# Performance work log

Measured on AMD Instinct MI355X. Metric: run time of the kernel, lower is better.

## Reference

```python
import jax, jax.numpy as jnp
import numpy as np

B, N, CIN, COUT = 4, 4096, 64, 64

def setup_inputs() -> dict:
    key = jax.random.key(0)
    k1, k2, k3, k4, k5 = jax.random.split(key, 5)
    X = jax.random.normal(k1, (B, N, CIN), dtype=jnp.float32)
    A = jax.random.uniform(k2, (N, N), dtype=jnp.float32)
    weight1 = jax.random.normal(k3, (CIN, COUT), dtype=jnp.float32) * 0.05
    weight2 = jax.random.normal(k4, (1 * COUT, COUT), dtype=jnp.float32) * 0.05
    alpha = jax.random.normal(k5, (2 * COUT, 1), dtype=jnp.float32) * 0.05
    return {"X": X, "A": A, "weight1": weight1, "weight2": weight2, "alpha": alpha}

def reference(X, A, weight1, weight2, alpha):
    n = A.shape[0]
    c = weight1.shape[1]
    b = X.shape[0]
    # add self loops on the adjacency diagonal
    idx = jnp.arange(n)
    adj = A.at[idx, idx].set(1.0)
    # node transform: [B,N,C]
    out = jnp.matmul(X, weight1)
    # edge feature (P=1): [N,N,1], row-normalized over j (axis=1)
    E = adj[:, :, None]
    E_wave = E / E.sum(axis=1, keepdims=True)
    # attention scores via rank-1 decomposition of alpha
    att_l = jnp.matmul(out, alpha[:c])   # [B,N,1]
    att_r = jnp.matmul(out, alpha[c:])   # [B,N,1]
    scores = jax.nn.leaky_relu(att_l @ jnp.swapaxes(att_r, 1, 2))  # [B,N,N]
    # exp + edge-feature weighting: [P,B,N,N]
    att = jnp.einsum('bij,ijp->pbij', jnp.exp(scores), E_wave)
    # manual softmax-style normalization over neighbors j
    att = att / att.sum(axis=-1, keepdims=True)
    # aggregate: [B,N,P,C] -> [B,N,P*C]
    agg = jnp.einsum('pbij,bjc->bipc', att, out).reshape(b, n, -1)
    return jnp.matmul(agg, weight2)
```

## Files before the change

kernel.cpp:

```cpp
#include <hip/hip_runtime.h>
#include <hip/hip_bf16.h>

typedef __attribute__((ext_vector_type(8))) short short8;
typedef __attribute__((ext_vector_type(4))) float floatx4;

#define NN 4096

static __device__ __forceinline__ unsigned f2bf_rne(float x) {
    union { float f; unsigned u; } v; v.f = x;
    unsigned r = v.u + 0x7fffu + ((v.u >> 16) & 1u);
    return r >> 16;
}
static __device__ __forceinline__ float bf2f(unsigned hi) {
    union { unsigned u; float f; } v; v.u = hi << 16; return v.f;
}

__global__ __launch_bounds__(256, 4)
void prep_kernel(const float* __restrict__ X,
                 const float* __restrict__ W1,
                 const float* __restrict__ W2,
                 const float* __restrict__ alpha,
                 unsigned short* __restrict__ Gt,
                 float* __restrict__ lv,
                 float* __restrict__ rv) {
    __shared__ __align__(16) char sm[53248];
    float* W1s  = (float*)sm;
    float* W2s  = (float*)(sm + 17408);
    float* Wcst = (float*)(sm + 34816);
    float* w1s  = (float*)(sm + 52224);
    float* als  = (float*)(sm + 52736);
    float* GsT  = (float*)sm;

    const int t = threadIdx.x;
    const int row0 = blockIdx.x * 64;
    const int b = row0 >> 12, n0 = row0 & (NN - 1);
    const int w = t >> 6, lane = t & 63;
    const int m = lane & 15, q = lane >> 4;

    const int row = row0 + w * 16 + m;
    const float* xp = X + (size_t)row * 64;
    float4 x0 = *(const float4*)(xp + q * 8);
    float4 x1 = *(const float4*)(xp + q * 8 + 4);
    float4 x2 = *(const float4*)(xp + 32 + q * 8);
    float4 x3 = *(const float4*)(xp + 32 + q * 8 + 4);

    #pragma unroll
    for (int s = 0; s < 4; ++s) {
        int idx = s * 1024 + t * 4;
        int r = idx >> 6, cc = idx & 63;
        *(float4*)&W1s[r * 68 + cc] = *(const float4*)(W1 + idx);
        *(float4*)&W2s[r * 68 + cc] = *(const float4*)(W2 + idx);
    }
    if (t < 128) als[t] = alpha[t];
    __syncthreads();

    {
        const int k = t >> 2, nq = t & 3;
        float acc[16];
        #pragma unroll
        for (int i = 0; i < 16; ++i) acc[i] = 0.f;
        for (int mm = 0; mm < 64; ++mm) {
            float w1v = W1s[k * 68 + mm];
            #pragma unroll
            for (int i = 0; i < 16; ++i)
                acc[i] += w1v * W2s[mm * 68 + nq * 16 + i];
        }
        #pragma unroll
        for (int i = 0; i < 16; ++i)
            Wcst[(nq * 16 + i) * 68 + k] = acc[i];
    }
    if (t < 64) {
        float sl = 0.f, sr = 0.f;
        for (int cc2 = 0; cc2 < 64; ++cc2) {
            float wv = W1s[t * 68 + cc2];
            sl += wv * als[cc2];
            sr += wv * als[64 + cc2];
        }
        w1s[t] = sl; w1s[64 + t] = sr;
    }
    __syncthreads();

    const float xs[16] = {x0.x,x0.y,x0.z,x0.w, x1.x,x1.y,x1.z,x1.w,
                          x2.x,x2.y,x2.z,x2.w, x3.x,x3.y,x3.z,x3.w};

    float pl = 0.f, pr = 0.f;
    #pragma unroll
    for (int ks = 0; ks < 2; ++ks)
        #pragma unroll
        for (int j = 0; j < 8; ++j) {
            int k = ks * 32 + q * 8 + j;
            float xv = xs[ks * 8 + j];
            pl += xv * w1s[k];
            pr += xv * w1s[64 + k];
        }
    pl += __shfl_xor(pl, 16, 64); pl += __shfl_xor(pl, 32, 64);
    pr += __shfl_xor(pr, 16, 64); pr += __shfl_xor(pr, 32, 64);
    if (q == 0) { lv[row] = pl; rv[row] = pr; }

    short8 ah[2], al[2];
    #pragma unroll
    for (int ks = 0; ks < 2; ++ks)
        #pragma unroll
        for (int j = 0; j < 8; ++j) {
            float f = xs[ks * 8 + j];
            unsigned hb = f2bf_rne(f);
            float res = f - bf2f(hb);
            ah[ks][j] = (short)hb;
            al[ks][j] = (short)f2bf_rne(res);
        }

    short8 bfr[4][2];
    #pragma unroll
    for (int nt = 0; nt < 4; ++nt)
        #pragma unroll
        for (int ks = 0; ks < 2; ++ks) {
            const float* wp = &Wcst[(nt * 16 + m) * 68 + ks * 32 + q * 8];
            float4 w0 = *(const float4*)wp;
            float4 w1 = *(const float4*)(wp + 4);
            short8 bf;
            bf[0] = (short)f2bf_rne(w0.x); bf[1] = (short)f2bf_rne(w0.y);
            bf[2] = (short)f2bf_rne(w0.z); bf[3] = (short)f2bf_rne(w0.w);
            bf[4] = (short)f2bf_rne(w1.x); bf[5] = (short)f2bf_rne(w1.y);
            bf[6] = (short)f2bf_rne(w1.z); bf[7] = (short)f2bf_rne(w1.w);
            bfr[nt][ks] = bf;
        }

    floatx4 acc[4] = {{0,0,0,0},{0,0,0,0},{0,0,0,0},{0,0,0,0}};
    #pragma unroll
    for (int ks = 0; ks < 2; ++ks)
        #pragma unroll
        for (int nt = 0; nt < 4; ++nt) {
            acc[nt] = __builtin_amdgcn_mfma_f32_16x16x32_bf16(ah[ks], bfr[nt][ks], acc[nt], 0, 0, 0);
            acc[nt] = __builtin_amdgcn_mfma_f32_16x16x32_bf16(al[ks], bfr[nt][ks], acc[nt], 0, 0, 0);
        }

    __syncthreads();
    #pragma unroll
    for (int nt = 0; nt < 4; ++nt)
        #pragma unroll
        for (int rg = 0; rg < 4; ++rg)
            GsT[(nt * 16 + m) * 68 + w * 16 + q * 4 + rg] = acc[nt][rg];
    __syncthreads();
    unsigned* Gu = (unsigned*)Gt;
    #pragma unroll
    for (int it2 = 0; it2 < 8; ++it2) {
        int c2 = (t >> 5) + it2 * 8;
        int np = t & 31;
        unsigned lo = f2bf_rne(GsT[c2 * 68 + 2 * np]);
        unsigned hi = f2bf_rne(GsT[c2 * 68 + 2 * np + 1]);
        Gu[(((((size_t)(b * 64 + c2)) << 12) + n0) >> 1) + np] = lo | (hi << 16);
    }
}

__global__ __launch_bounds__(1024, 4)
void attn_kernel(const float* __restrict__ A,
                 const unsigned short* __restrict__ Gt,
                 const float* __restrict__ lv,
                 const float* __restrict__ rv,
                 float* __restrict__ out) {
    __shared__ __align__(16) char sm[57600];
    float* rs = (float*)sm;
    float* lis = (float*)(sm + 16384);
    unsigned short* Es = (unsigned short*)(sm + 16640);
    unsigned short* Gs = (unsigned short*)(sm + 37120);

    const int bx = blockIdx.x;
    const int i0 = (bx & 63) * 64;
    const int b  = bx >> 6;
    const int t = threadIdx.x;
    const int wave = t >> 6, lane = t & 63;
    const int grp = wave >> 2, wsub = wave & 3;
    const int m = lane & 15, q = lane >> 4;
    const int irow = wsub * 16 + (lane >> 2);
    const int jseg = lane & 3;

    *(float4*)&rs[t * 4] = *(const float4*)(rv + b * NN + t * 4);
    if (t < 64) lis[t] = lv[b * NN + i0 + t] * 1.44269504f;

    const float* aRow = A + (size_t)(i0 + irow) * NN + grp * 1024 + jseg * 8;
    const unsigned short* gRow = Gt + (((size_t)(b * 64 + irow)) << 12) + grp * 1024 + jseg * 8;
    const int jd = (i0 + irow) - grp * 1024;
    const bool diag_grp = (((i0 + irow) >> 10) == grp);

    unsigned short* EsG = Es + grp * 2560;
    unsigned short* GsG = Gs + grp * 2560;

    float4 a0A = *(const float4*)(aRow);
    float4 a1A = *(const float4*)(aRow + 4);
    uint4  gA  = *(const uint4*)(gRow);
    float4 a0B = *(const float4*)(aRow + 32);
    float4 a1B = *(const float4*)(aRow + 36);
    uint4  gB  = *(const uint4*)(gRow + 32);

    __syncthreads();
    const float li = lis[irow];

    floatx4 acc0 = {0,0,0,0}, acc1 = {0,0,0,0}, acc2 = {0,0,0,0},
            acc3 = {0,0,0,0}, accd = {0,0,0,0};
    short8 ones;
    #pragma unroll
    for (int e = 0; e < 8; ++e) ones[e] = (short)0x3F80;

    auto genE = [&](float4 a0, float4 a1, int chunk) -> uint4 {
        const int jl = chunk * 32 + jseg * 8;
        float aa[8] = {a0.x, a0.y, a0.z, a0.w, a1.x, a1.y, a1.z, a1.w};
        if (diag_grp && (jd >> 5) == chunk) {
            const int dd = jd - jl;
            #pragma unroll
            for (int e = 0; e < 8; ++e) if (dd == e) aa[e] = 1.0f;
        }
        const float4 r0 = *(const float4*)&rs[grp * 1024 + jl];
        const float4 r1 = *(const float4*)&rs[grp * 1024 + jl + 4];
        const float rr[8] = {r0.x, r0.y, r0.z, r0.w, r1.x, r1.y, r1.z, r1.w};
        unsigned ew[4];
        #pragma unroll
        for (int e2 = 0; e2 < 4; ++e2) {
            float s0 = li * rr[2 * e2], s1 = li * rr[2 * e2 + 1];
            s0 = fmaxf(s0, 0.01f * s0);
            s1 = fmaxf(s1, 0.01f * s1);
            float e0 = exp2f(s0) * aa[2 * e2];
            float e1 = exp2f(s1) * aa[2 * e2 + 1];
            ew[e2] = __builtin_amdgcn_perm(__float_as_uint(e1) + 0x8000u,
                                           __float_as_uint(e0) + 0x8000u, 0x07060302u);
        }
        return uint4{ew[0], ew[1], ew[2], ew[3]};
    };

    const int eoff = irow * 40 + jseg * 8;
    for (int c = 0; c < 32; c += 2) {
        uint4 eA = genE(a0A, a1A, c);
        uint4 gsvA = gA;
        { int jn = (c + 2 < 32) ? (c + 2) * 32 : c * 32;
          a0A = *(const float4*)(aRow + jn);
          a1A = *(const float4*)(aRow + jn + 4);
          gA  = *(const uint4*)(gRow + jn); }
        __syncthreads();
        *(uint4*)&EsG[eoff] = eA;
        *(uint4*)&GsG[eoff] = gsvA;
        __syncthreads();
        {
            short8 afr = *(const short8*)&EsG[(wsub * 16 + m) * 40 + q * 8];
            short8 b0  = *(const short8*)&GsG[(m)      * 40 + q * 8];
            short8 b1  = *(const short8*)&GsG[(16 + m) * 40 + q * 8];
            short8 b2  = *(const short8*)&GsG[(32 + m) * 40 + q * 8];
            short8 b3  = *(const short8*)&GsG[(48 + m) * 40 + q * 8];
            acc0 = __builtin_amdgcn_mfma_f32_16x16x32_bf16(afr, b0, acc0, 0, 0, 0);
            acc1 = __builtin_amdgcn_mfma_f32_16x16x32_bf16(afr, b1, acc1, 0, 0, 0);
            acc2 = __builtin_amdgcn_mfma_f32_16x16x32_bf16(afr, b2, acc2, 0, 0, 0);
            acc3 = __builtin_amdgcn_mfma_f32_16x16x32_bf16(afr, b3, acc3, 0, 0, 0);
            accd = __builtin_amdgcn_mfma_f32_16x16x32_bf16(afr, ones, accd, 0, 0, 0);
        }
        uint4 eB = genE(a0B, a1B, c + 1);
        uint4 gsvB = gB;
        { int jn = (c + 3 < 32) ? (c + 3) * 32 : (c + 1) * 32;
          a0B = *(const float4*)(aRow + jn);
          a1B = *(const float4*)(aRow + jn + 4);
          gB  = *(const uint4*)(gRow + jn); }
        __syncthreads();
        *(uint4*)&EsG[eoff] = eB;
        *(uint4*)&GsG[eoff] = gsvB;
        __syncthreads();
        {
            short8 afr = *(const short8*)&EsG[(wsub * 16 + m) * 40 + q * 8];
            short8 b0  = *(const short8*)&GsG[(m)      * 40 + q * 8];
            short8 b1  = *(const short8*)&GsG[(16 + m) * 40 + q * 8];
            short8 b2  = *(const short8*)&GsG[(32 + m) * 40 + q * 8];
            short8 b3  = *(const short8*)&GsG[(48 + m) * 40 + q * 8];
            acc0 = __builtin_amdgcn_mfma_f32_16x16x32_bf16(afr, b0, acc0, 0, 0, 0);
            acc1 = __builtin_amdgcn_mfma_f32_16x16x32_bf16(afr, b1, acc1, 0, 0, 0);
            acc2 = __builtin_amdgcn_mfma_f32_16x16x32_bf16(afr, b2, acc2, 0, 0, 0);
            acc3 = __builtin_amdgcn_mfma_f32_16x16x32_bf16(afr, b3, acc3, 0, 0, 0);
            accd = __builtin_amdgcn_mfma_f32_16x16x32_bf16(afr, ones, accd, 0, 0, 0);
        }
    }

    __syncthreads();
    float* red = (float*)sm;
    const int il = t >> 4, c4 = t & 15;
    float4 osum = {0.f, 0.f, 0.f, 0.f};
    float dsum = 0.f;
    #pragma unroll
    for (int pass = 0; pass < 2; ++pass) {
        if ((grp >> 1) == pass) {
            float* rp_ = red + (grp & 1) * 4352;
            #pragma unroll
            for (int nt = 0; nt < 4; ++nt) {
                floatx4 av = nt == 0 ? acc0 : nt == 1 ? acc1 : nt == 2 ? acc2 : acc3;
                #pragma unroll
                for (int rg = 0; rg < 4; ++rg)
                    rp_[(wsub * 16 + q * 4 + rg) * 68 + nt * 16 + m] = av[rg];
            }
            if (m == 0) {
                #pragma unroll
                for (int rg = 0; rg < 4; ++rg)
                    rp_[(wsub * 16 + q * 4 + rg) * 68 + 64] = accd[rg];
            }
        }
        __syncthreads();
        {
            float4 v0 = *(const float4*)&red[il * 68 + c4 * 4];
            float4 v1 = *(const float4*)&red[4352 + il * 68 + c4 * 4];
            osum.x += v0.x + v1.x; osum.y += v0.y + v1.y;
            osum.z += v0.z + v1.z; osum.w += v0.w + v1.w;
            dsum += red[il * 68 + 64] + red[4352 + il * 68 + 64];
        }
        __syncthreads();
    }
    const float rinv = 1.0f / dsum;
    float4 o;
    o.x = osum.x * rinv; o.y = osum.y * rinv;
    o.z = osum.z * rinv; o.w = osum.w * rinv;
    *(float4*)(out + (((size_t)(b * NN + i0 + il)) << 6) + c4 * 4) = o;
}

extern "C" void kernel_launch(void* const* d_in, const int* in_sizes, int n_in,
                              void* d_out, int out_size, void* d_ws, size_t ws_size,
                              hipStream_t stream) {
    const float* X     = (const float*)d_in[0];
    const float* A     = (const float*)d_in[1];
    const float* W1    = (const float*)d_in[2];
    const float* W2    = (const float*)d_in[3];
    const float* alpha = (const float*)d_in[4];
    float* out = (float*)d_out;

    char* ws = (char*)d_ws;
    unsigned short* Gt = (unsigned short*)(ws);
    float* lvp = (float*)(ws + 2097152);
    float* rvp = (float*)(ws + 2097152 + 65536);

    prep_kernel<<<256, 256, 0, stream>>>(X, W1, W2, alpha, Gt, lvp, rvp);
    attn_kernel<<<256, 1024, 0, stream>>>(A, Gt, lvp, rvp, out);
}
```

Baseline: 149.4 us.

## Load E fragments directly in registers, stream G via async LDS loads

The attention kernel now builds the exp-weighted adjacency fragment directly in MFMA A-operand layout in registers, which removes the LDS round trip for E and one barrier per chunk. The G tiles are streamed into a 4-deep LDS ring with global_load_lds, so copies no longer pass through registers. The row-sum is accumulated on the VALU from the rounded bf16 values instead of a separate MFMA against a ones vector. The W1·W2 and W1·alpha products are hoisted out of every prep block into a one-block precompute kernel, which adds a launch and a serial dependency.

```diff
diff --git a/kernel.cpp b/kernel.cpp
--- a/kernel.cpp
+++ b/kernel.cpp
@@ -3,6 +3,7 @@
 
 typedef __attribute__((ext_vector_type(8))) short short8;
 typedef __attribute__((ext_vector_type(4))) float floatx4;
+typedef unsigned int u32;
 
 #define NN 4096
 
@@ -15,20 +16,65 @@
     union { unsigned u; float f; } v; v.u = hi << 16; return v.f;
 }
 
+static __device__ __forceinline__ void gld16(void* l, const void* g) {
+    __builtin_amdgcn_global_load_lds(
+        (const __attribute__((address_space(1))) u32*)g,
+        (__attribute__((address_space(3))) u32*)l, 16, 0, 0);
+}
+
+__global__ __launch_bounds__(256, 1)
+void wc_kernel(const float* __restrict__ W1,
+               const float* __restrict__ W2,
+               const float* __restrict__ alpha,
+               float* __restrict__ WcstG,
+               float* __restrict__ w1aG) {
+    __shared__ __align__(16) float W1s[64 * 68];
+    __shared__ __align__(16) float W2s[64 * 68];
+    __shared__ float als[128];
+    const int t = threadIdx.x;
+    #pragma unroll
+    for (int s = 0; s < 4; ++s) {
+        int idx = s * 1024 + t * 4;
+        int r = idx >> 6, cc = idx & 63;
+        *(float4*)&W1s[r * 68 + cc] = *(const float4*)(W1 + idx);
+        *(float4*)&W2s[r * 68 + cc] = *(const float4*)(W2 + idx);
+    }
+    if (t < 128) als[t] = alpha[t];
+    __syncthreads();
+    const int k = t >> 2, nq = t & 3;
+    float acc[16];
+    #pragma unroll
+    for (int i = 0; i < 16; ++i) acc[i] = 0.f;
+    for (int mm = 0; mm < 64; ++mm) {
+        float w1v = W1s[k * 68 + mm];
+        #pragma unroll
+        for (int i = 0; i < 16; ++i)
+            acc[i] += w1v * W2s[mm * 68 + nq * 16 + i];
+    }
+    #pragma unroll
+    for (int i = 0; i < 16; ++i)
+        WcstG[(nq * 16 + i) * 68 + k] = acc[i];
+    if (t < 64) {
+        float sl = 0.f, sr = 0.f;
+        for (int cc2 = 0; cc2 < 64; ++cc2) {
+            float wv = W1s[t * 68 + cc2];
+            sl += wv * als[cc2];
+            sr += wv * als[64 + cc2];
+        }
+        w1aG[t] = sl; w1aG[64 + t] = sr;
+    }
+}
+
 __global__ __launch_bounds__(256, 4)
 void prep_kernel(const float* __restrict__ X,
-                 const float* __restrict__ W1,
-                 const float* __restrict__ W2,
-                 const float* __restrict__ alpha,
+                 const float* __restrict__ WcstG,
+                 const float* __restrict__ w1aG,
                  unsigned short* __restrict__ Gt,
                  float* __restrict__ lv,
                  float* __restrict__ rv) {
-    __shared__ __align__(16) char sm[53248];
-    float* W1s  = (float*)sm;
-    float* W2s  = (float*)(sm + 17408);
-    float* Wcst = (float*)(sm + 34816);
-    float* w1s  = (float*)(sm + 52224);
-    float* als  = (float*)(sm + 52736);
+    __shared__ __align__(16) char sm[17920];
+    float* Wcst = (float*)sm;
+    float* w1s  = (float*)(sm + 17408);
     float* GsT  = (float*)sm;
 
     const int t = threadIdx.x;
@@ -45,39 +91,11 @@
     float4 x3 = *(const float4*)(xp + 32 + q * 8 + 4);
 
     #pragma unroll
-    for (int s = 0; s < 4; ++s) {
-        int idx = s * 1024 + t * 4;
-        int r = idx >> 6, cc = idx & 63;
-        *(float4*)&W1s[r * 68 + cc] = *(const float4*)(W1 + idx);
-        *(float4*)&W2s[r * 68 + cc] = *(const float4*)(W2 + idx);
-    }
-    if (t < 128) als[t] = alpha[t];
-    __syncthreads();
-
-    {
-        const int k = t >> 2, nq = t & 3;
-        float acc[16];
-        #pragma unroll
-        for (int i = 0; i < 16; ++i) acc[i] = 0.f;
-        for (int mm = 0; mm < 64; ++mm) {
-            float w1v = W1s[k * 68 + mm];
-            #pragma unroll
-            for (int i = 0; i < 16; ++i)
-                acc[i] += w1v * W2s[mm * 68 + nq * 16 + i];
-        }
-        #pragma unroll
-        for (int i = 0; i < 16; ++i)
-            Wcst[(nq * 16 + i) * 68 + k] = acc[i];
-    }
-    if (t < 64) {
-        float sl = 0.f, sr = 0.f;
-        for (int cc2 = 0; cc2 < 64; ++cc2) {
-            float wv = W1s[t * 68 + cc2];
-            sl += wv * als[cc2];
-            sr += wv * als[64 + cc2];
-        }
-        w1s[t] = sl; w1s[64 + t] = sr;
-    }
+    for (int it = 0; it < 5; ++it) {
+        int i = it * 1024 + t * 4;
+        if (i < 4352) *(float4*)&Wcst[i] = *(const float4*)(WcstG + i);
+    }
+    if (t < 128) w1s[t] = w1aG[t];
     __syncthreads();
 
     const float xs[16] = {x0.x,x0.y,x0.z,x0.w, x1.x,x1.y,x1.z,x1.w,
@@ -158,11 +176,7 @@
                  const float* __restrict__ lv,
                  const float* __restrict__ rv,
                  float* __restrict__ out) {
-    __shared__ __align__(16) char sm[57600];
-    float* rs = (float*)sm;
-    float* lis = (float*)(sm + 16384);
-    unsigned short* Es = (unsigned short*)(sm + 16640);
-    unsigned short* Gs = (unsigned short*)(sm + 37120);
+    __shared__ __align__(16) char sm[65536];
 
     const int bx = blockIdx.x;
     const int i0 = (bx & 63) * 64;
@@ -171,114 +185,85 @@
     const int wave = t >> 6, lane = t & 63;
     const int grp = wave >> 2, wsub = wave & 3;
     const int m = lane & 15, q = lane >> 4;
-    const int irow = wsub * 16 + (lane >> 2);
-    const int jseg = lane & 3;
-
-    *(float4*)&rs[t * 4] = *(const float4*)(rv + b * NN + t * 4);
-    if (t < 64) lis[t] = lv[b * NN + i0 + t] * 1.44269504f;
-
-    const float* aRow = A + (size_t)(i0 + irow) * NN + grp * 1024 + jseg * 8;
-    const unsigned short* gRow = Gt + (((size_t)(b * 64 + irow)) << 12) + grp * 1024 + jseg * 8;
+    const int irow = wsub * 16 + m;
+
+    const float* aRow = A + (size_t)(i0 + irow) * NN + grp * 1024 + q * 8;
+    const unsigned short* gRow = Gt + (((size_t)(b * 64 + irow)) << 12) + grp * 1024 + q * 8;
+    const float* rvg = rv + (size_t)b * NN + grp * 1024 + q * 8;
+    char* gdst = sm + grp * 4096 + wsub * 1024;
+
+    const float li = lv[b * NN + i0 + irow] * 1.44269504f;
+    const float li001 = li * 0.01f;
+
+    gld16(gdst, gRow);
+    float4 a0 = *(const float4*)(aRow);
+    float4 a1 = *(const float4*)(aRow + 4);
+    float4 r0 = *(const float4*)(rvg);
+    float4 r1 = *(const float4*)(rvg + 4);
+
+    const bool diag_grp = ((i0 >> 10) == grp);
     const int jd = (i0 + irow) - grp * 1024;
-    const bool diag_grp = (((i0 + irow) >> 10) == grp);
-
-    unsigned short* EsG = Es + grp * 2560;
-    unsigned short* GsG = Gs + grp * 2560;
-
-    float4 a0A = *(const float4*)(aRow);
-    float4 a1A = *(const float4*)(aRow + 4);
-    uint4  gA  = *(const uint4*)(gRow);
-    float4 a0B = *(const float4*)(aRow + 32);
-    float4 a1B = *(const float4*)(aRow + 36);
-    uint4  gB  = *(const uint4*)(gRow + 32);
-
-    __syncthreads();
-    const float li = lis[irow];
-
-    floatx4 acc0 = {0,0,0,0}, acc1 = {0,0,0,0}, acc2 = {0,0,0,0},
-            acc3 = {0,0,0,0}, accd = {0,0,0,0};
-    short8 ones;
-    #pragma unroll
-    for (int e = 0; e < 8; ++e) ones[e] = (short)0x3F80;
-
-    auto genE = [&](float4 a0, float4 a1, int chunk) -> uint4 {
-        const int jl = chunk * 32 + jseg * 8;
+
+    floatx4 acc0 = {0,0,0,0}, acc1 = {0,0,0,0}, acc2 = {0,0,0,0}, acc3 = {0,0,0,0};
+    float dsum = 0.f;
+
+    unsigned short* Gbuf = (unsigned short*)sm;
+
+    #pragma unroll 4
+    for (int cc = 0; cc < 32; ++cc) {
+        if (cc < 31) gld16(gdst + ((cc + 1) & 3) * 16384, gRow + (cc + 1) * 32);
+
         float aa[8] = {a0.x, a0.y, a0.z, a0.w, a1.x, a1.y, a1.z, a1.w};
-        if (diag_grp && (jd >> 5) == chunk) {
-            const int dd = jd - jl;
+        if (diag_grp && ((jd >> 5) == cc)) {
+            const int dd = jd - (cc * 32 + q * 8);
             #pragma unroll
             for (int e = 0; e < 8; ++e) if (dd == e) aa[e] = 1.0f;
         }
-        const float4 r0 = *(const float4*)&rs[grp * 1024 + jl];
-        const float4 r1 = *(const float4*)&rs[grp * 1024 + jl + 4];
         const float rr[8] = {r0.x, r0.y, r0.z, r0.w, r1.x, r1.y, r1.z, r1.w};
-        unsigned ew[4];
-        #pragma unroll
-        for (int e2 = 0; e2 < 4; ++e2) {
-            float s0 = li * rr[2 * e2], s1 = li * rr[2 * e2 + 1];
-            s0 = fmaxf(s0, 0.01f * s0);
-            s1 = fmaxf(s1, 0.01f * s1);
-            float e0 = exp2f(s0) * aa[2 * e2];
-            float e1 = exp2f(s1) * aa[2 * e2 + 1];
-            ew[e2] = __builtin_amdgcn_perm(__float_as_uint(e1) + 0x8000u,
-                                           __float_as_uint(e0) + 0x8000u, 0x07060302u);
-        }
-        return uint4{ew[0], ew[1], ew[2], ew[3]};
-    };
-
-    const int eoff = irow * 40 + jseg * 8;
-    for (int c = 0; c < 32; c += 2) {
-        uint4 eA = genE(a0A, a1A, c);
-        uint4 gsvA = gA;
-        { int jn = (c + 2 < 32) ? (c + 2) * 32 : c * 32;
-          a0A = *(const float4*)(aRow + jn);
-          a1A = *(const float4*)(aRow + jn + 4);
-          gA  = *(const uint4*)(gRow + jn); }
-        __syncthreads();
-        *(uint4*)&EsG[eoff] = eA;
-        *(uint4*)&GsG[eoff] = gsvA;
+        unsigned up[8];
+        #pragma unroll
+        for (int e = 0; e < 8; ++e) {
+            float s = fmaxf(li * rr[e], li001 * rr[e]);
+            float ev = __builtin_amdgcn_exp2f(s) * aa[e];
+            unsigned u = __float_as_uint(ev) + 0x8000u;
+            up[e] = u;
+            dsum += __uint_as_float(u & 0xffff0000u);
+        }
+        union { unsigned u[4]; short8 s8; } cv;
+        cv.u[0] = __builtin_amdgcn_perm(up[1], up[0], 0x07060302u);
+        cv.u[1] = __builtin_amdgcn_perm(up[3], up[2], 0x07060302u);
+        cv.u[2] = __builtin_amdgcn_perm(up[5], up[4], 0x07060302u);
+        cv.u[3] = __builtin_amdgcn_perm(up[7], up[6], 0x07060302u);
+        const short8 afr = cv.s8;
+
+        { const int jn = (cc < 31) ? (cc + 1) * 32 : 0;
+          a0 = *(const float4*)(aRow + jn);
+          a1 = *(const float4*)(aRow + jn + 4);
+          r0 = *(const float4*)(rvg + jn);
+          r1 = *(const float4*)(rvg + jn + 4); }
+
         __syncthreads();
         {
-            short8 afr = *(const short8*)&EsG[(wsub * 16 + m) * 40 + q * 8];
-            short8 b0  = *(const short8*)&GsG[(m)      * 40 + q * 8];
-            short8 b1  = *(const short8*)&GsG[(16 + m) * 40 + q * 8];
-            short8 b2  = *(const short8*)&GsG[(32 + m) * 40 + q * 8];
-            short8 b3  = *(const short8*)&GsG[(48 + m) * 40 + q * 8];
+            const unsigned short* Gb = Gbuf + (cc & 3) * 8192 + grp * 2048;
+            const short8 b0 = *(const short8*)&Gb[lane * 8];
+            const short8 b1 = *(const short8*)&Gb[512 + lane * 8];
+            const short8 b2 = *(const short8*)&Gb[1024 + lane * 8];
+            const short8 b3 = *(const short8*)&Gb[1536 + lane * 8];
             acc0 = __builtin_amdgcn_mfma_f32_16x16x32_bf16(afr, b0, acc0, 0, 0, 0);
             acc1 = __builtin_amdgcn_mfma_f32_16x16x32_bf16(afr, b1, acc1, 0, 0, 0);
             acc2 = __builtin_amdgcn_mfma_f32_16x16x32_bf16(afr, b2, acc2, 0, 0, 0);
             acc3 = __builtin_amdgcn_mfma_f32_16x16x32_bf16(afr, b3, acc3, 0, 0, 0);
-            accd = __builtin_amdgcn_mfma_f32_16x16x32_bf16(afr, ones, accd, 0, 0, 0);
-        }
-        uint4 eB = genE(a0B, a1B, c + 1);
-        uint4 gsvB = gB;
-        { int jn = (c + 3 < 32) ? (c + 3) * 32 : (c + 1) * 32;
-          a0B = *(const float4*)(aRow + jn);
-          a1B = *(const float4*)(aRow + jn + 4);
-          gB  = *(const uint4*)(gRow + jn); }
-        __syncthreads();
-        *(uint4*)&EsG[eoff] = eB;
-        *(uint4*)&GsG[eoff] = gsvB;
-        __syncthreads();
-        {
-            short8 afr = *(const short8*)&EsG[(wsub * 16 + m) * 40 + q * 8];
-            short8 b0  = *(const short8*)&GsG[(m)      * 40 + q * 8];
-            short8 b1  = *(const short8*)&GsG[(16 + m) * 40 + q * 8];
-            short8 b2  = *(const short8*)&GsG[(32 + m) * 40 + q * 8];
-            short8 b3  = *(const short8*)&GsG[(48 + m) * 40 + q * 8];
-            acc0 = __builtin_amdgcn_mfma_f32_16x16x32_bf16(afr, b0, acc0, 0, 0, 0);
-            acc1 = __builtin_amdgcn_mfma_f32_16x16x32_bf16(afr, b1, acc1, 0, 0, 0);
-            acc2 = __builtin_amdgcn_mfma_f32_16x16x32_bf16(afr, b2, acc2, 0, 0, 0);
-            acc3 = __builtin_amdgcn_mfma_f32_16x16x32_bf16(afr, b3, acc3, 0, 0, 0);
-            accd = __builtin_amdgcn_mfma_f32_16x16x32_bf16(afr, ones, accd, 0, 0, 0);
-        }
-    }
+        }
+    }
+
+    dsum += __shfl_xor(dsum, 16, 64);
+    dsum += __shfl_xor(dsum, 32, 64);
 
     __syncthreads();
     float* red = (float*)sm;
     const int il = t >> 4, c4 = t & 15;
     float4 osum = {0.f, 0.f, 0.f, 0.f};
-    float dsum = 0.f;
+    float dtot = 0.f;
     #pragma unroll
     for (int pass = 0; pass < 2; ++pass) {
         if ((grp >> 1) == pass) {
@@ -290,11 +275,7 @@
                 for (int rg = 0; rg < 4; ++rg)
                     rp_[(wsub * 16 + q * 4 + rg) * 68 + nt * 16 + m] = av[rg];
             }
-            if (m == 0) {
-                #pragma unroll
-                for (int rg = 0; rg < 4; ++rg)
-                    rp_[(wsub * 16 + q * 4 + rg) * 68 + 64] = accd[rg];
-            }
+            if (q == 0) rp_[(wsub * 16 + m) * 68 + 64] = dsum;
         }
         __syncthreads();
         {
@@ -302,11 +283,11 @@
             float4 v1 = *(const float4*)&red[4352 + il * 68 + c4 * 4];
             osum.x += v0.x + v1.x; osum.y += v0.y + v1.y;
             osum.z += v0.z + v1.z; osum.w += v0.w + v1.w;
-            dsum += red[il * 68 + 64] + red[4352 + il * 68 + 64];
+            dtot += red[il * 68 + 64] + red[4352 + il * 68 + 64];
         }
         __syncthreads();
     }
-    const float rinv = 1.0f / dsum;
+    const float rinv = 1.0f / dtot;
     float4 o;
     o.x = osum.x * rinv; o.y = osum.y * rinv;
     o.z = osum.z * rinv; o.w = osum.w * rinv;
@@ -325,9 +306,12 @@
 
     char* ws = (char*)d_ws;
     unsigned short* Gt = (unsigned short*)(ws);
-    float* lvp = (float*)(ws + 2097152);
-    float* rvp = (float*)(ws + 2097152 + 65536);
-
-    prep_kernel<<<256, 256, 0, stream>>>(X, W1, W2, alpha, Gt, lvp, rvp);
+    float* lvp   = (float*)(ws + 2097152);
+    float* rvp   = (float*)(ws + 2097152 + 65536);
+    float* WcstG = (float*)(ws + 2097152 + 131072);
+    float* w1aG  = (float*)(ws + 2097152 + 131072 + 17408);
+
+    wc_kernel<<<1, 256, 0, stream>>>(W1, W2, alpha, WcstG, w1aG);
+    prep_kernel<<<256, 256, 0, stream>>>(X, WcstG, w1aG, Gt, lvp, rvp);
     attn_kernel<<<256, 1024, 0, stream>>>(A, Gt, lvp, rvp, out);
 }
```

Result: slower. 175.1 us (+17.2%).
